# Kernel optimization log

Hardware: AMD Instinct MI355X
Metric: run time of the kernel (lower is better)

## Reference

```python
import jax, jax.numpy as jnp
import numpy as np

D_MODEL = 1024
NUM_HEADS = 16
D_K = D_MODEL // NUM_HEADS


def setup_inputs() -> dict:
    key = jax.random.key(0)
    ks = jax.random.split(key, 9)
    s = 1.0 / np.sqrt(D_MODEL)
    return {
        "z": jax.random.normal(ks[0], (4, 2048, D_MODEL), dtype=jnp.float32),
        "Wq": jax.random.uniform(ks[1], (D_MODEL, D_MODEL), jnp.float32, -s, s),
        "bq": jax.random.uniform(ks[2], (D_MODEL,), jnp.float32, -s, s),
        "Wk": jax.random.uniform(ks[3], (D_MODEL, D_MODEL), jnp.float32, -s, s),
        "bk": jax.random.uniform(ks[4], (D_MODEL,), jnp.float32, -s, s),
        "Wv": jax.random.uniform(ks[5], (D_MODEL, D_MODEL), jnp.float32, -s, s),
        "bv": jax.random.uniform(ks[6], (D_MODEL,), jnp.float32, -s, s),
        "Wo": jax.random.uniform(ks[7], (D_MODEL, D_MODEL), jnp.float32, -s, s),
        "bo": jax.random.uniform(ks[8], (D_MODEL,), jnp.float32, -s, s),
    }


def reference(z, Wq, bq, Wk, bk, Wv, bv, Wo, bo):
    B, S, _ = z.shape
    # project and split heads: [B, H, S, d_k]
    def proj(W, b):
        return (z @ W.T + b).reshape(B, S, NUM_HEADS, D_K).transpose(0, 2, 1, 3)
    Q, K, V = proj(Wq, bq), proj(Wk, bk), proj(Wv, bv)
    scale = 1.0 / np.sqrt(D_K)
    scores = jnp.einsum('bhqd,bhkd->bhqk', Q, K) * scale
    probs = jax.nn.softmax(scores, axis=-1)
    ctx = jnp.einsum('bhqk,bhkd->bhqd', probs, V)
    ctx = ctx.transpose(0, 2, 1, 3).reshape(B, S, D_MODEL)
    return ctx @ Wo.T + bo
```

## Files before the change

kernel.cpp:

```cpp
#include <hip/hip_runtime.h>
#include <stdint.h>

#define D_MODEL 1024
#define NHEAD 16
#define DKH 64
#define BATCH 4
#define SEQ 2048
#define M_ROWS (BATCH*SEQ)
#define NBH (BATCH*NHEAD)

typedef float f32x4 __attribute__((ext_vector_type(4)));
typedef __bf16 bf16x8 __attribute__((ext_vector_type(8)));
typedef __bf16 bf16x4v __attribute__((ext_vector_type(4)));
typedef short short4v __attribute__((ext_vector_type(4)));

__device__ __forceinline__ unsigned short f2bf(float x) {
    __bf16 b = (__bf16)x;
    return __builtin_bit_cast(unsigned short, b);
}

#define GLL(gsrc, ldst) \
    __builtin_amdgcn_global_load_lds((const __attribute__((address_space(1))) void*)(gsrc), \
                                     (__attribute__((address_space(3))) void*)(ldst), 16, 0, 0)

__global__ __launch_bounds__(256) void k_convert(
    const float* __restrict__ z,  const float* __restrict__ wq,
    const float* __restrict__ wk, const float* __restrict__ wv,
    const float* __restrict__ wo,
    const float* __restrict__ bq, const float* __restrict__ bk,
    const float* __restrict__ bv,
    unsigned short* __restrict__ zb, unsigned short* __restrict__ wqkv,
    unsigned short* __restrict__ wob, float* __restrict__ biasf)
{
    int i = blockIdx.x * 256 + threadIdx.x;
    {
        float4 v = ((const float4*)z)[i];
        ushort4 o; o.x = f2bf(v.x); o.y = f2bf(v.y); o.z = f2bf(v.z); o.w = f2bf(v.w);
        ((ushort4*)zb)[i] = o;
    }
    if (i < 262144) {
        float4 v;
        ushort4 o;
        v = ((const float4*)wq)[i];
        o.x=f2bf(v.x); o.y=f2bf(v.y); o.z=f2bf(v.z); o.w=f2bf(v.w);
        ((ushort4*)wqkv)[i] = o;
        v = ((const float4*)wk)[i];
        o.x=f2bf(v.x); o.y=f2bf(v.y); o.z=f2bf(v.z); o.w=f2bf(v.w);
        ((ushort4*)wqkv)[262144 + i] = o;
        v = ((const float4*)wv)[i];
        o.x=f2bf(v.x); o.y=f2bf(v.y); o.z=f2bf(v.z); o.w=f2bf(v.w);
        ((ushort4*)wqkv)[524288 + i] = o;
        v = ((const float4*)wo)[i];
        o.x=f2bf(v.x); o.y=f2bf(v.y); o.z=f2bf(v.z); o.w=f2bf(v.w);
        ((ushort4*)wob)[i] = o;
    }
    if (i < 1024) {
        biasf[i]        = bq[i];
        biasf[1024 + i] = bk[i];
        biasf[2048 + i] = bv[i];
    }
}

__global__ __launch_bounds__(256) void k_gemm_qkv(
    const unsigned short* __restrict__ A,
    const unsigned short* __restrict__ Bw,
    const float* __restrict__ biasf,
    unsigned short* __restrict__ qb, unsigned short* __restrict__ kb,
    unsigned short* __restrict__ vtb)
{
    __shared__ unsigned short lds_a[128 * 32];
    __shared__ unsigned short lds_b[128 * 32];

    const int NT = 3072 / 128;
    int bid = blockIdx.x;
    int tn = bid % NT, tm = bid / NT;
    int m0 = tm * 128, n0 = tn * 128;
    int tid = threadIdx.x, wid = tid >> 6, lane = tid & 63;
    int wm = wid >> 1, wn = wid & 1;

    f32x4 acc[4][4] = {};

    int srow = lane >> 2;
    int scol = (lane & 3) * 8;

    for (int kt = 0; kt < 32; ++kt) {
        int k0 = kt * 32;
#pragma unroll
        for (int i = 0; i < 2; ++i) {
            int rb = (wid * 2 + i) * 16;
            GLL(A  + (size_t)(m0 + rb + srow) * 1024 + k0 + scol, lds_a + rb * 32);
            GLL(Bw + (size_t)(n0 + rb + srow) * 1024 + k0 + scol, lds_b + rb * 32);
        }
        __syncthreads();
        bf16x8 af[4], bfr[4];
#pragma unroll
        for (int i = 0; i < 4; ++i)
            af[i] = *(const bf16x8*)(lds_a + (wm * 64 + i * 16 + (lane & 15)) * 32 + (lane >> 4) * 8);
#pragma unroll
        for (int j = 0; j < 4; ++j)
            bfr[j] = *(const bf16x8*)(lds_b + (wn * 64 + j * 16 + (lane & 15)) * 32 + (lane >> 4) * 8);
#pragma unroll
        for (int i = 0; i < 4; ++i)
#pragma unroll
            for (int j = 0; j < 4; ++j)
                acc[i][j] = __builtin_amdgcn_mfma_f32_16x16x32_bf16(af[i], bfr[j], acc[i][j], 0, 0, 0);
        __syncthreads();
    }

    int t = n0 >> 10;
#pragma unroll
    for (int j = 0; j < 4; ++j) {
        int col = n0 + wn * 64 + j * 16 + (lane & 15);
        float bias = biasf[col];
        int d  = col & 1023;
        int h  = d >> 6;
        int dk = d & 63;
#pragma unroll
        for (int i = 0; i < 4; ++i) {
#pragma unroll
            for (int r = 0; r < 4; ++r) {
                int row = m0 + wm * 64 + i * 16 + (lane >> 4) * 4 + r;
                float v = acc[i][j][r] + bias;
                unsigned short bv16 = f2bf(v);
                int b_ = row >> 11, s_ = row & 2047;
                int bh = b_ * NHEAD + h;
                if (t == 0)      qb[((size_t)bh * SEQ + s_) * DKH + dk] = bv16;
                else if (t == 1) kb[((size_t)bh * SEQ + s_) * DKH + dk] = bv16;
                else             vtb[((size_t)bh * DKH + dk) * SEQ + s_] = bv16;
            }
        }
    }
}

__device__ __forceinline__ void stage_kv(
    const unsigned short* __restrict__ kb, const unsigned short* __restrict__ vtb,
    unsigned short* lk, unsigned short* lv,
    int bh, int t, int wid, int srow8, int sc)
{
#pragma unroll
    for (int i = 0; i < 2; ++i) {
        int rb = wid * 16 + i * 8;
        int row = rb + srow8;
        int cs = (sc ^ (row & 7)) * 8;
        GLL(kb  + ((size_t)bh * SEQ + t * 64 + row) * DKH + cs, lk + rb * 64);
        GLL(vtb + ((size_t)bh * DKH + row) * SEQ + t * 64 + cs, lv + rb * 64);
    }
}

__global__ __launch_bounds__(256) void k_attn(
    const unsigned short* __restrict__ qg,
    const unsigned short* __restrict__ kb,
    const unsigned short* __restrict__ vtb,
    unsigned short* __restrict__ ctxb)
{
    __shared__ unsigned short lds_k[2][64 * 64];
    __shared__ unsigned short lds_v[2][64 * 64];

    int bid = blockIdx.x;
    int x = bid & 7, li = bid >> 3;
    int bh = x * 8 + (li >> 4);
    int qt = li & 15;

    int tid = threadIdx.x, wid = tid >> 6, lane = tid & 63;
    int lq = lane & 15, g = lane >> 4;
    int srow8 = lane >> 3, sc = lane & 7;

    bf16x8 aq[2][2];
    {
        const unsigned short* qp = qg + ((size_t)bh * SEQ + qt * 128 + wid * 32 + lq) * DKH + g * 8;
        aq[0][0] = *(const bf16x8*)(qp);
        aq[0][1] = *(const bf16x8*)(qp + 32);
        aq[1][0] = *(const bf16x8*)(qp + 16 * DKH);
        aq[1][1] = *(const bf16x8*)(qp + 16 * DKH + 32);
    }

    float m2[2]   = { -1e30f, -1e30f };
    float lsum[2] = { 0.f, 0.f };
    f32x4 oacc[2][4] = {};

    const float SC = 0.125f;
    const float THR = 8.0f;

    stage_kv(kb, vtb, &lds_k[0][0], &lds_v[0][0], bh, 0, wid, srow8, sc);

    for (int kt = 0; kt < 32; ++kt) {
        int cur = kt & 1;
        if (kt < 31) {
            stage_kv(kb, vtb, &lds_k[cur ^ 1][0], &lds_v[cur ^ 1][0], bh, kt + 1, wid, srow8, sc);
            asm volatile("s_waitcnt vmcnt(4)" ::: "memory");
        } else {
            asm volatile("s_waitcnt vmcnt(0)" ::: "memory");
        }
        __builtin_amdgcn_s_barrier();

        f32x4 st[2][4] = {};
#pragma unroll
        for (int kk = 0; kk < 2; ++kk) {
            bf16x8 kf[4];
#pragma unroll
            for (int jb = 0; jb < 4; ++jb) {
                int row = jb * 16 + lq;
                int c = kk * 4 + g;
                kf[jb] = *(const bf16x8*)(&lds_k[cur][row * 64 + ((c ^ (row & 7)) * 8)]);
            }
#pragma unroll
            for (int jb = 0; jb < 4; ++jb)
#pragma unroll
                for (int q = 0; q < 2; ++q)
                    st[q][jb] = __builtin_amdgcn_mfma_f32_16x16x32_bf16(kf[jb], aq[q][kk], st[q][jb], 0, 0, 0);
        }

        float mt[2];
        bool need = false;
#pragma unroll
        for (int q = 0; q < 2; ++q) {
            float a0 = fmaxf(fmaxf(st[q][0][0], st[q][0][1]), fmaxf(st[q][0][2], st[q][0][3]));
            float a1 = fmaxf(fmaxf(st[q][1][0], st[q][1][1]), fmaxf(st[q][1][2], st[q][1][3]));
            float a2 = fmaxf(fmaxf(st[q][2][0], st[q][2][1]), fmaxf(st[q][2][2], st[q][2][3]));
            float a3 = fmaxf(fmaxf(st[q][3][0], st[q][3][1]), fmaxf(st[q][3][2], st[q][3][3]));
            float t0 = fmaxf(fmaxf(a0, a1), fmaxf(a2, a3));
            t0 = fmaxf(t0, __shfl_xor(t0, 16));
            t0 = fmaxf(t0, __shfl_xor(t0, 32));
            mt[q] = t0 * SC;
            need = need || (mt[q] > m2[q] + THR);
        }
        if (__any(need)) {
#pragma unroll
            for (int q = 0; q < 2; ++q) {
                float mn = fmaxf(m2[q], mt[q]);
                float alpha = __expf(m2[q] - mn);
                m2[q] = mn;
                lsum[q] *= alpha;
#pragma unroll
                for (int dj = 0; dj < 4; ++dj) {
                    oacc[q][dj][0] *= alpha; oacc[q][dj][1] *= alpha;
                    oacc[q][dj][2] *= alpha; oacc[q][dj][3] *= alpha;
                }
            }
        }

        short4v w[2][4];
#pragma unroll
        for (int q = 0; q < 2; ++q) {
            float s = 0.f;
#pragma unroll
            for (int jb = 0; jb < 4; ++jb) {
                float p0 = __expf(st[q][jb][0] * SC - m2[q]);
                float p1 = __expf(st[q][jb][1] * SC - m2[q]);
                float p2 = __expf(st[q][jb][2] * SC - m2[q]);
                float p3 = __expf(st[q][jb][3] * SC - m2[q]);
                s += (p0 + p1) + (p2 + p3);
                bf16x4v pb;
                pb[0] = (__bf16)p0; pb[1] = (__bf16)p1; pb[2] = (__bf16)p2; pb[3] = (__bf16)p3;
                w[q][jb] = __builtin_bit_cast(short4v, pb);
            }
            s += __shfl_xor(s, 16);
            s += __shfl_xor(s, 32);
            lsum[q] += s;
        }

#pragma unroll
        for (int dj = 0; dj < 4; ++dj) {
            int row = dj * 16 + lq;
            int rx = row & 7;
#pragma unroll
            for (int jb = 0; jb < 4; ++jb) {
                int c = jb * 2 + (g >> 1);
                short4v vf = *(const short4v*)(&lds_v[cur][row * 64 + ((c ^ rx) * 8) + (g & 1) * 4]);
#pragma unroll
                for (int q = 0; q < 2; ++q)
                    oacc[q][dj] = __builtin_amdgcn_mfma_f32_16x16x16bf16_1k(vf, w[q][jb], oacc[q][dj], 0, 0, 0);
            }
        }
        __builtin_amdgcn_s_barrier();
    }

    int b_ = bh >> 4, h = bh & 15;
#pragma unroll
    for (int q = 0; q < 2; ++q) {
        float inv = 1.0f / lsum[q];
        int s_ = qt * 128 + wid * 32 + q * 16 + lq;
        unsigned short* op = ctxb + (((size_t)b_ * SEQ + s_) * NHEAD + h) * DKH;
#pragma unroll
        for (int dj = 0; dj < 4; ++dj) {
#pragma unroll
            for (int t = 0; t < 2; ++t) {
                unsigned short e0 = f2bf(oacc[q][dj][2 * t]     * inv);
                unsigned short e1 = f2bf(oacc[q][dj][2 * t + 1] * inv);
                unsigned int u = ((unsigned int)e1 << 16) | (unsigned int)e0;
                *(unsigned int*)(op + dj * 16 + 4 * g + 2 * t) = u;
            }
        }
    }
}

__global__ __launch_bounds__(256) void k_gemm_out(
    const unsigned short* __restrict__ A,
    const unsigned short* __restrict__ Bw,
    const float* __restrict__ bo,
    float* __restrict__ out)
{
    __shared__ unsigned short lds_a[128 * 32];
    __shared__ unsigned short lds_b[128 * 32];

    const int NT = 1024 / 128;
    int bid = blockIdx.x;
    int tn = bid % NT, tm = bid / NT;
    int m0 = tm * 128, n0 = tn * 128;
    int tid = threadIdx.x, wid = tid >> 6, lane = tid & 63;
    int wm = wid >> 1, wn = wid & 1;

    f32x4 acc[4][4] = {};

    int srow = lane >> 2;
    int scol = (lane & 3) * 8;

    for (int kt = 0; kt < 32; ++kt) {
        int k0 = kt * 32;
#pragma unroll
        for (int i = 0; i < 2; ++i) {
            int rb = (wid * 2 + i) * 16;
            GLL(A  + (size_t)(m0 + rb + srow) * 1024 + k0 + scol, lds_a + rb * 32);
            GLL(Bw + (size_t)(n0 + rb + srow) * 1024 + k0 + scol, lds_b + rb * 32);
        }
        __syncthreads();
        bf16x8 af[4], bfr[4];
#pragma unroll
        for (int i = 0; i < 4; ++i)
            af[i] = *(const bf16x8*)(lds_a + (wm * 64 + i * 16 + (lane & 15)) * 32 + (lane >> 4) * 8);
#pragma unroll
        for (int j = 0; j < 4; ++j)
            bfr[j] = *(const bf16x8*)(lds_b + (wn * 64 + j * 16 + (lane & 15)) * 32 + (lane >> 4) * 8);
#pragma unroll
        for (int i = 0; i < 4; ++i)
#pragma unroll
            for (int j = 0; j < 4; ++j)
                acc[i][j] = __builtin_amdgcn_mfma_f32_16x16x32_bf16(af[i], bfr[j], acc[i][j], 0, 0, 0);
        __syncthreads();
    }

#pragma unroll
    for (int j = 0; j < 4; ++j) {
        int col = n0 + wn * 64 + j * 16 + (lane & 15);
        float bias = bo[col];
#pragma unroll
        for (int i = 0; i < 4; ++i) {
#pragma unroll
            for (int r = 0; r < 4; ++r) {
                int row = m0 + wm * 64 + i * 16 + (lane >> 4) * 4 + r;
                out[(size_t)row * 1024 + col] = acc[i][j][r] + bias;
            }
        }
    }
}

extern "C" void kernel_launch(void* const* d_in, const int* in_sizes, int n_in,
                              void* d_out, int out_size, void* d_ws, size_t ws_size,
                              hipStream_t stream)
{
    const float* z  = (const float*)d_in[0];
    const float* Wq = (const float*)d_in[1];
    const float* bq = (const float*)d_in[2];
    const float* Wk = (const float*)d_in[3];
    const float* bk = (const float*)d_in[4];
    const float* Wv = (const float*)d_in[5];
    const float* bv = (const float*)d_in[6];
    const float* Wo = (const float*)d_in[7];
    const float* bo = (const float*)d_in[8];
    float* out = (float*)d_out;

    char* ws = (char*)d_ws;
    unsigned short* zb   = (unsigned short*)(ws);
    unsigned short* ctxb = (unsigned short*)(ws);
    unsigned short* wqkv = (unsigned short*)(ws + (16ull << 20));
    unsigned short* wob  = (unsigned short*)(ws + (22ull << 20));
    float*          biasf= (float*)(ws + (24ull << 20));
    unsigned short* qb   = (unsigned short*)(ws + (25ull << 20));
    unsigned short* kb   = (unsigned short*)(ws + (41ull << 20));
    unsigned short* vtb  = (unsigned short*)(ws + (57ull << 20));

    k_convert<<<8192, 256, 0, stream>>>(z, Wq, Wk, Wv, Wo, bq, bk, bv, zb, wqkv, wob, biasf);
    k_gemm_qkv<<<64 * 24, 256, 0, stream>>>(zb, wqkv, biasf, qb, kb, vtb);
    k_attn<<<NBH * 16, 256, 0, stream>>>(qb, kb, vtb, ctxb);
    k_gemm_out<<<64 * 8, 256, 0, stream>>>(ctxb, wob, bo, out);
}
```

Baseline: 256.9 us.

## Use 16x16x32 MFMA for PV product via permlane-transposed P fragments

Replaces the PV product's 16x16x16 bf16 MFMAs with 16x16x32 MFMAs, halving the MFMA instruction count and using 128-bit LDS reads of V. The P tile is repacked across lanes with permlane32_swap and shfl_xor so it can serve as the A operand. This swaps the output orientation, so alpha rescaling and the final 1/l normalisation now fetch per-row values with shuffles, and the output is written as scattered 16-bit stores. The aim is higher MFMA throughput in the inner loop, at the cost of extra cross-lane shuffles and less coalesced output stores.

```diff
diff --git a/kernel.cpp b/kernel.cpp
--- a/kernel.cpp
+++ b/kernel.cpp
@@ -11,8 +11,8 @@
 
 typedef float f32x4 __attribute__((ext_vector_type(4)));
 typedef __bf16 bf16x8 __attribute__((ext_vector_type(8)));
-typedef __bf16 bf16x4v __attribute__((ext_vector_type(4)));
-typedef short short4v __attribute__((ext_vector_type(4)));
+typedef int int2v __attribute__((ext_vector_type(2)));
+typedef int int4v __attribute__((ext_vector_type(4)));
 
 __device__ __forceinline__ unsigned short f2bf(float x) {
     __bf16 b = (__bf16)x;
@@ -164,6 +164,7 @@
     int tid = threadIdx.x, wid = tid >> 6, lane = tid & 63;
     int lq = lane & 15, g = lane >> 4;
     int srow8 = lane >> 3, sc = lane & 7;
+    bool gOdd = (g & 1) != 0;
 
     bf16x8 aq[2][2];
     {
@@ -225,21 +226,28 @@
             need = need || (mt[q] > m2[q] + THR);
         }
         if (__any(need)) {
+            float alpha[2];
 #pragma unroll
             for (int q = 0; q < 2; ++q) {
                 float mn = fmaxf(m2[q], mt[q]);
-                float alpha = __expf(m2[q] - mn);
+                alpha[q] = __expf(m2[q] - mn);
                 m2[q] = mn;
-                lsum[q] *= alpha;
+                lsum[q] *= alpha[q];
+            }
+#pragma unroll
+            for (int q = 0; q < 2; ++q) {
+                f32x4 ar;
+#pragma unroll
+                for (int r = 0; r < 4; ++r) ar[r] = __shfl(alpha[q], 4 * g + r);
 #pragma unroll
                 for (int dj = 0; dj < 4; ++dj) {
-                    oacc[q][dj][0] *= alpha; oacc[q][dj][1] *= alpha;
-                    oacc[q][dj][2] *= alpha; oacc[q][dj][3] *= alpha;
+                    oacc[q][dj][0] *= ar[0]; oacc[q][dj][1] *= ar[1];
+                    oacc[q][dj][2] *= ar[2]; oacc[q][dj][3] *= ar[3];
                 }
             }
         }
 
-        short4v w[2][4];
+        unsigned int pk[2][4][2];
 #pragma unroll
         for (int q = 0; q < 2; ++q) {
             float s = 0.f;
@@ -250,26 +258,48 @@
                 float p2 = __expf(st[q][jb][2] * SC - m2[q]);
                 float p3 = __expf(st[q][jb][3] * SC - m2[q]);
                 s += (p0 + p1) + (p2 + p3);
-                bf16x4v pb;
-                pb[0] = (__bf16)p0; pb[1] = (__bf16)p1; pb[2] = (__bf16)p2; pb[3] = (__bf16)p3;
-                w[q][jb] = __builtin_bit_cast(short4v, pb);
+                pk[q][jb][0] = (unsigned int)f2bf(p0) | ((unsigned int)f2bf(p1) << 16);
+                pk[q][jb][1] = (unsigned int)f2bf(p2) | ((unsigned int)f2bf(p3) << 16);
             }
             s += __shfl_xor(s, 16);
             s += __shfl_xor(s, 32);
             lsum[q] += s;
         }
 
+        bf16x8 paf[2][2];
+#pragma unroll
+        for (int q = 0; q < 2; ++q) {
+#pragma unroll
+            for (int kk = 0; kk < 2; ++kk) {
+                int a0 = (int)pk[q][2 * kk][0],     a1 = (int)pk[q][2 * kk][1];
+                int b0 = (int)pk[q][2 * kk + 1][0], b1 = (int)pk[q][2 * kk + 1][1];
+                int2v r0 = __builtin_amdgcn_permlane32_swap(a0, b0, false, false);
+                int2v r1 = __builtin_amdgcn_permlane32_swap(a1, b1, false, false);
+                int c0 = gOdd ? r0[1] : r0[0];
+                int c1 = gOdd ? r1[1] : r1[0];
+                int e0 = gOdd ? r0[0] : r0[1];
+                int e1 = gOdd ? r1[0] : r1[1];
+                int s0 = __shfl_xor(e0, 16);
+                int s1 = __shfl_xor(e1, 16);
+                int4v ti;
+                ti[0] = gOdd ? s0 : c0;
+                ti[1] = gOdd ? s1 : c1;
+                ti[2] = gOdd ? c0 : s0;
+                ti[3] = gOdd ? c1 : s1;
+                paf[q][kk] = __builtin_bit_cast(bf16x8, ti);
+            }
+        }
+
 #pragma unroll
         for (int dj = 0; dj < 4; ++dj) {
             int row = dj * 16 + lq;
             int rx = row & 7;
 #pragma unroll
-            for (int jb = 0; jb < 4; ++jb) {
-                int c = jb * 2 + (g >> 1);
-                short4v vf = *(const short4v*)(&lds_v[cur][row * 64 + ((c ^ rx) * 8) + (g & 1) * 4]);
+            for (int kk = 0; kk < 2; ++kk) {
+                bf16x8 vf = *(const bf16x8*)(&lds_v[cur][row * 64 + (((kk * 4 + g) ^ rx) * 8)]);
 #pragma unroll
                 for (int q = 0; q < 2; ++q)
-                    oacc[q][dj] = __builtin_amdgcn_mfma_f32_16x16x16bf16_1k(vf, w[q][jb], oacc[q][dj], 0, 0, 0);
+                    oacc[q][dj] = __builtin_amdgcn_mfma_f32_16x16x32_bf16(paf[q][kk], vf, oacc[q][dj], 0, 0, 0);
             }
         }
         __builtin_amdgcn_s_barrier();
@@ -278,17 +308,19 @@
     int b_ = bh >> 4, h = bh & 15;
 #pragma unroll
     for (int q = 0; q < 2; ++q) {
-        float inv = 1.0f / lsum[q];
-        int s_ = qt * 128 + wid * 32 + q * 16 + lq;
-        unsigned short* op = ctxb + (((size_t)b_ * SEQ + s_) * NHEAD + h) * DKH;
+        f32x4 linv;
+#pragma unroll
+        for (int r = 0; r < 4; ++r) linv[r] = __shfl(lsum[q], 4 * g + r);
+#pragma unroll
+        for (int r = 0; r < 4; ++r) linv[r] = 1.0f / linv[r];
+        int sbase = qt * 128 + wid * 32 + q * 16 + 4 * g;
 #pragma unroll
         for (int dj = 0; dj < 4; ++dj) {
 #pragma unroll
-            for (int t = 0; t < 2; ++t) {
-                unsigned short e0 = f2bf(oacc[q][dj][2 * t]     * inv);
-                unsigned short e1 = f2bf(oacc[q][dj][2 * t + 1] * inv);
-                unsigned int u = ((unsigned int)e1 << 16) | (unsigned int)e0;
-                *(unsigned int*)(op + dj * 16 + 4 * g + 2 * t) = u;
+            for (int r = 0; r < 4; ++r) {
+                int s_ = sbase + r;
+                ctxb[(((size_t)b_ * SEQ + s_) * NHEAD + h) * DKH + dj * 16 + lq] =
+                    f2bf(oacc[q][dj][r] * linv[r]);
             }
         }
     }
```

Result: slower. 266.8 us (+3.9%).
